# Kernel tuning notes

Measured on AMD Instinct MI355X. Metric: run time of the kernel, lower is better.

The kernel has to match this reference:

```python
import jax, jax.numpy as jnp
import numpy as np

NUM_QUBITS = 21
NUM_LAYERS = 4
ACTION_DIM = 18
STATE_DIM = 2 ** NUM_QUBITS  # amplitude register size


def _rx(t):
    c = jnp.cos(t / 2)
    s = jnp.sin(t / 2)
    return jnp.stack([jnp.stack([c + 0j, -1j * s]), jnp.stack([-1j * s, c + 0j])]).astype(jnp.complex64)


def _ry(t):
    c = jnp.cos(t / 2)
    s = jnp.sin(t / 2)
    return jnp.stack([jnp.stack([c, -s]), jnp.stack([s, c])]).astype(jnp.complex64)


def _rz(t):
    e = jnp.exp(-1j * t / 2).astype(jnp.complex64)
    z = jnp.zeros_like(e)
    return jnp.stack([jnp.stack([e, z]), jnp.stack([z, jnp.conj(e)])])


def apply_1q(psi, U, q):
    # wire 0 is the most-significant bit (PennyLane convention)
    s = psi.reshape(2 ** q, 2, -1)
    s = jnp.einsum('ab,xbz->xaz', U, s)
    return s.reshape(-1)


def apply_cnot(psi, c, t):
    a, b = (c, t) if c < t else (t, c)
    s = psi.reshape(2 ** a, 2, 2 ** (b - a - 1), 2, -1)
    ctrl_ax = 1 if c < t else 3
    tgt_ax = 3 if c < t else 1
    s0 = jax.lax.index_in_dim(s, 0, axis=ctrl_ax, keepdims=False)
    s1 = jax.lax.index_in_dim(s, 1, axis=ctrl_ax, keepdims=False)
    tgt_in_slab = tgt_ax if tgt_ax < ctrl_ax else tgt_ax - 1
    s1 = jnp.flip(s1, axis=tgt_in_slab)  # X on target where control==1
    s = jnp.stack([s0, s1], axis=ctrl_ax)
    return s.reshape(-1)


def _layer(psi, lp, entangle):
    # lp: (NUM_QUBITS, 3) rotation angles for this layer
    for q in range(NUM_QUBITS):
        psi = apply_1q(psi, _rx(lp[q, 0]), q)
        psi = apply_1q(psi, _ry(lp[q, 1]), q)
        psi = apply_1q(psi, _rz(lp[q, 2]), q)
    if entangle:
        for q in range(NUM_QUBITS - 1):
            psi = apply_cnot(psi, q, q + 1)
        psi = apply_cnot(psi, NUM_QUBITS - 1, 0)
    return psi


def setup_inputs() -> dict:
    key = jax.random.key(0)
    k1, k2, k3, k4 = jax.random.split(key, 4)
    state = jax.random.normal(k1, (STATE_DIM,), dtype=jnp.float32)
    circuit_params = jax.random.normal(k2, (NUM_LAYERS * NUM_QUBITS * 3,), dtype=jnp.float32) * 0.01
    bound = 1.0 / np.sqrt(NUM_QUBITS)
    head_w = jax.random.uniform(k3, (ACTION_DIM, NUM_QUBITS), jnp.float32, -bound, bound)
    head_b = jax.random.uniform(k4, (ACTION_DIM,), jnp.float32, -bound, bound)
    return {'state': state, 'circuit_params': circuit_params, 'head_w': head_w, 'head_b': head_b}


def reference(state, circuit_params, head_w, head_b):
    # Amplitude encoding: normalize (state_dim == 2**num_qubits so no padding needed)
    norm = jnp.linalg.norm(state)
    inv = jnp.where(norm > 0, 1.0 / jnp.maximum(norm, 1e-30), 0.0)
    basis0 = jnp.zeros((STATE_DIM,), jnp.float32).at[0].set(1.0)
    amp = jnp.where(norm > 0, state * inv, basis0)
    psi = amp.astype(jnp.complex64)

    lp = circuit_params.reshape(NUM_LAYERS, NUM_QUBITS, 3)
    for layer in range(NUM_LAYERS):
        psi = _layer(psi, lp[layer], layer < NUM_LAYERS - 1)

    # Pauli-Z expectation values per qubit from |psi|^2
    probs = psi.real ** 2 + psi.imag ** 2
    zvals = []
    for q in range(NUM_QUBITS):
        p = probs.reshape(2 ** q, 2, -1)
        zvals.append(p[:, 0, :].sum() - p[:, 1, :].sum())
    meas = jnp.stack(zvals).astype(jnp.float32)

    logits = head_w @ meas + head_b
    return jax.nn.softmax(logits, axis=-1)
```

## Files before the change

### kernel.cpp

```cpp
#include <hip/hip_runtime.h>

#define NQ 21
#define DIM (1 << NQ)
#define NL 4
#define ADIM 18
#define GBA 512
#define GBB 256
#define NT 512

__device__ __forceinline__ float2 cfma2(float2 u0, float2 a, float2 u1, float2 b) {
    return make_float2(u0.x * a.x - u0.y * a.y + u1.x * b.x - u1.y * b.y,
                       u0.x * a.y + u0.y * a.x + u1.x * b.y + u1.y * b.x);
}

struct GateU { float2 u00, u01, u10, u11; };

__device__ __forceinline__ void bfly(float2& a, float2& b, const GateU& U) {
    float2 na = cfma2(U.u00, a, U.u01, b);
    float2 nb = cfma2(U.u10, a, U.u11, b);
    a = na; b = nb;
}

__device__ __forceinline__ int sw(int j) { return j ^ (((j >> 4) & 7) << 1); }

__device__ __forceinline__ void make_mats(GateU* mats, const float* __restrict__ cp, int layer, int tid) {
    if (tid < NQ) {
        const float* ang = cp + (layer * NQ + tid) * 3;
        float a = ang[0], b = ang[1], c = ang[2];
        float ca = cosf(0.5f * a), sa = sinf(0.5f * a);
        float cb = cosf(0.5f * b), sb = sinf(0.5f * b);
        float cc = cosf(0.5f * c), sc = sinf(0.5f * c);
        float2 m00 = make_float2(cb * ca,  sb * sa);
        float2 m01 = make_float2(-sb * ca, -cb * sa);
        float2 m10 = make_float2(sb * ca,  -cb * sa);
        float2 m11 = make_float2(cb * ca,  -sb * sa);
        GateU U;
        U.u00 = make_float2(cc * m00.x + sc * m00.y, cc * m00.y - sc * m00.x);
        U.u01 = make_float2(cc * m01.x + sc * m01.y, cc * m01.y - sc * m01.x);
        U.u10 = make_float2(cc * m10.x - sc * m10.y, cc * m10.y + sc * m10.x);
        U.u11 = make_float2(cc * m11.x - sc * m11.y, cc * m11.y + sc * m11.x);
        mats[tid] = U;
    }
}

__device__ __forceinline__ void round3(float2* tile, int tid, int g,
                                       GateU Ua, GateU Ub, GateU Uc) {
    int bl = (1 << g) - 1;
    int base = (tid & bl) | ((tid >> g) << (g + 3));
    float2 v[8];
#pragma unroll
    for (int j = 0; j < 8; ++j) v[j] = tile[sw(base + (j << g))];
#pragma unroll
    for (int s = 0; s < 8; s += 2) bfly(v[s], v[s + 1], Ua);
#pragma unroll
    for (int s = 0; s < 8; ++s) if (!(s & 2)) bfly(v[s], v[s | 2], Ub);
#pragma unroll
    for (int s = 0; s < 8; ++s) if (!(s & 4)) bfly(v[s], v[s | 4], Uc);
#pragma unroll
    for (int j = 0; j < 8; ++j) tile[sw(base + (j << g))] = v[j];
    __syncthreads();
}

__global__ __launch_bounds__(NT, 4) void k_passB(const float* __restrict__ state,
                                                 float2* __restrict__ psi,
                                                 const float* __restrict__ cp, int layer) {
    __shared__ float2 tile[4096];
    __shared__ GateU mats[NQ];
    const int tid = threadIdx.x, blk = blockIdx.x;
    float4* psi4 = (float4*)psi;

    make_mats(mats, cp, layer, tid);
    const int srcmask = (layer < 3) ? 0xFF : 0;

    for (int H = 0; H < 2; ++H) {
        if (H) __syncthreads();
        if (layer == 0) {
            const float4* s4 = (const float4*)state;
            for (int i = 0; i < 2; ++i) {
                int f = i * NT + tid;
                int d = f & 1, h = f >> 1;
                float4 w = s4[(h << 10) | (blk << 2) | (2 * H + d)];
                int s = (h << 3) | (4 * d);
                tile[sw(s)]     = make_float2(w.x, 0.f);
                tile[sw(s + 1)] = make_float2(w.y, 0.f);
                tile[sw(s + 2)] = make_float2(w.z, 0.f);
                tile[sw(s + 3)] = make_float2(w.w, 0.f);
            }
        } else {
            for (int i = 0; i < 4; ++i) {
                int f = i * NT + tid;
                int c = f & 3, h = f >> 2;
                float4 w = psi4[(h << 11) | (blk << 3) | (4 * H + c)];
                int se = (h << 3) | (2 * c);
                tile[sw(se)]            = make_float2(w.x, w.y);
                tile[sw((se + 1) ^ 2048)] = make_float2(w.z, w.w);
            }
        }
        __syncthreads();
        round3(tile, tid, 3, mats[8], mats[7], mats[6]);
        round3(tile, tid, 6, mats[5], mats[4], mats[3]);
        round3(tile, tid, 9, mats[2], mats[1], mats[0]);
        for (int i = 0; i < 4; ++i) {
            int f = i * NT + tid;
            int c = f & 3, h = f >> 2;
            int hs = h ^ ((h >> 1) & srcmask);
            int s = (hs << 3) | (2 * c);
            float2 e0 = tile[sw(s)], e1 = tile[sw(s + 1)];
            psi4[(h << 11) | (blk << 3) | (4 * H + c)] = make_float4(e0.x, e0.y, e1.x, e1.y);
        }
    }
}

__global__ __launch_bounds__(NT, 4) void k_passA(float2* __restrict__ psi,
                                                 const float* __restrict__ cp, int layer,
                                                 float* __restrict__ partials) {
    __shared__ float2 tile[4096];
    __shared__ GateU mats[NQ];
    const int tid = threadIdx.x, blk = blockIdx.x;
    float4* psi4 = (float4*)psi;
    float4* t4 = (float4*)tile;

    {
        const float4* ga = psi4 + (size_t)blk * 2048;
        float2 v[8];
        float4 w[4];
        for (int i = 0; i < 4; ++i) w[i] = ga[i * NT + tid];
        make_mats(mats, cp, layer, tid);
        __syncthreads();
#pragma unroll
        for (int i = 0; i < 4; ++i) {
            v[2 * i]     = make_float2(w[i].x, w[i].y);
            v[2 * i + 1] = make_float2(w[i].z, w[i].w);
        }
        GateU U20 = mats[20];
#pragma unroll
        for (int s = 0; s < 8; s += 2) bfly(v[s], v[s + 1], U20);
        GateU U10 = mats[10];
#pragma unroll
        for (int s = 0; s < 8; ++s) if (!(s & 2)) bfly(v[s], v[s | 2], U10);
        GateU U9 = mats[9];
#pragma unroll
        for (int s = 0; s < 8; ++s) if (!(s & 4)) bfly(v[s], v[s | 4], U9);
        for (int i = 0; i < 4; ++i)
            t4[sw(2 * (i * NT + tid)) >> 1] =
                make_float4(v[2 * i].x, v[2 * i].y, v[2 * i + 1].x, v[2 * i + 1].y);
    }
    __syncthreads();
    round3(tile, tid, 1, mats[19], mats[18], mats[17]);
    round3(tile, tid, 4, mats[16], mats[15], mats[14]);
    round3(tile, tid, 7, mats[13], mats[12], mats[11]);

    if (layer < 3) {
        float4* oa = psi4 + (size_t)blk * 2048;
        int cb = (blk & 1) << 11;
        for (int i = 0; i < 4; ++i) {
            int f = i * NT + tid;
            int s0 = ((2 * f) ^ (f & 0x7FF)) ^ cb;
            float2 e0 = tile[sw(s0)], e1 = tile[sw(s0 ^ 1)];
            oa[f] = make_float4(e0.x, e0.y, e1.x, e1.y);
        }
    } else {
        float tot = 0.f, ones[NQ];
#pragma unroll
        for (int q = 0; q < NQ; ++q) ones[q] = 0.f;
        for (int it = 0; it < 8; ++it) {
            int j = it * NT + tid;
            float2 a2 = tile[sw(j)];
            float pr = a2.x * a2.x + a2.y * a2.y;
            int gidx = (blk << 12) | j;
            tot += pr;
#pragma unroll
            for (int q = 0; q < NQ; ++q)
                ones[q] += pr * (float)((gidx >> (20 - q)) & 1);
        }
        for (int off = 32; off; off >>= 1) {
            tot += __shfl_down(tot, off, 64);
#pragma unroll
            for (int q = 0; q < NQ; ++q) ones[q] += __shfl_down(ones[q], off, 64);
        }
        __syncthreads();
        float* red = (float*)tile;
        int wv = tid >> 6, ln = tid & 63;
        if (ln == 0) {
            red[wv * 22 + 21] = tot;
#pragma unroll
            for (int q = 0; q < NQ; ++q) red[wv * 22 + q] = ones[q];
        }
        __syncthreads();
        if (tid < 22) {
            float s = 0.f;
            for (int wvi = 0; wvi < 8; ++wvi) s += red[wvi * 22 + tid];
            partials[blk * 22 + tid] = s;
        }
    }
}

__global__ __launch_bounds__(NT) void k_final(const float* __restrict__ partials,
                                              const float* __restrict__ head_w,
                                              const float* __restrict__ head_b,
                                              float* __restrict__ out) {
    __shared__ float red[640];
    __shared__ float meas[NQ];
    __shared__ float lg[ADIM];
    int tid = threadIdx.x;
    int col = tid % 22, grp = tid / 22;
    if (tid < 506) {
        float s = 0.f;
        for (int r = grp; r < GBA; r += 23) s += partials[r * 22 + col];
        red[grp * 22 + col] = s;
    }
    __syncthreads();
    if (tid < 22) {
        float t2 = 0.f;
        for (int g = 0; g < 23; ++g) t2 += red[g * 22 + tid];
        red[600 + tid] = t2;
    }
    __syncthreads();
    if (tid < NQ) {
        float tot = red[600 + 21];
        meas[tid] = (tot > 0.f) ? (1.f - 2.f * red[600 + tid] / tot) : 1.f;
    }
    __syncthreads();
    if (tid < ADIM) {
        float s2 = head_b[tid];
        for (int q = 0; q < NQ; ++q) s2 += head_w[tid * NQ + q] * meas[q];
        lg[tid] = s2;
    }
    __syncthreads();
    if (tid == 0) {
        float m = lg[0];
        for (int a = 1; a < ADIM; ++a) m = fmaxf(m, lg[a]);
        float ssum = 0.f;
        for (int a = 0; a < ADIM; ++a) ssum += expf(lg[a] - m);
        float inv = 1.f / ssum;
        for (int a = 0; a < ADIM; ++a) out[a] = expf(lg[a] - m) * inv;
    }
}

extern "C" void kernel_launch(void* const* d_in, const int* in_sizes, int n_in,
                              void* d_out, int out_size, void* d_ws, size_t ws_size,
                              hipStream_t stream) {
    const float* state   = (const float*)d_in[0];
    const float* cparams = (const float*)d_in[1];
    const float* head_w  = (const float*)d_in[2];
    const float* head_b  = (const float*)d_in[3];
    float* out = (float*)d_out;

    float2* psi      = (float2*)d_ws;
    float*  partials = (float*)((char*)d_ws + (size_t)DIM * 8);

    for (int layer = 0; layer < NL; ++layer) {
        k_passB<<<GBB, NT, 0, stream>>>(state, psi, cparams, layer);
        k_passA<<<GBA, NT, 0, stream>>>(psi, cparams, layer, partials);
    }
    k_final<<<1, NT, 0, stream>>>(partials, head_w, head_b, out);
}
```

Baseline: 214.9 us.

## Prefetch both halves into registers, double-buffer LDS, fuse final reduction via last-block

Both passes now issue all global loads for a block's two tiles up front and keep two shared-memory buffers. This lets the second tile's memory latency overlap the first tile's butterfly rounds, and pass A runs half as many blocks, each doing two tiles. The separate final softmax kernel is removed: the last block to finish, detected with an atomic counter and cache-bypassing stores and loads, performs the reduction and head. Shared memory per block doubles and occupancy drops to 2 blocks per CU, and a memset launch is added.

Result: faster. 197.6 us (-8.1%).

```diff
diff --git a/kernel.cpp b/kernel.cpp
--- a/kernel.cpp
+++ b/kernel.cpp
@@ -4,8 +4,7 @@
 #define DIM (1 << NQ)
 #define NL 4
 #define ADIM 18
-#define GBA 512
-#define GBB 256
+#define GB 256
 #define NT 512
 
 __device__ __forceinline__ float2 cfma2(float2 u0, float2 a, float2 u1, float2 b) {
@@ -22,6 +21,19 @@
 }
 
 __device__ __forceinline__ int sw(int j) { return j ^ (((j >> 4) & 7) << 1); }
+
+__device__ __forceinline__ void store4_sc(float* p, float v) {
+    asm volatile("global_store_dword %0, %1, off sc0 sc1" :: "v"(p), "v"(v) : "memory");
+}
+__device__ __forceinline__ float load_sc_f(const float* p) {
+    float r;
+    asm volatile("global_load_dword %0, %1, off sc0 sc1\n\ts_waitcnt vmcnt(0)"
+                 : "=v"(r) : "v"(p) : "memory");
+    return r;
+}
+__device__ __forceinline__ void drain_vmem() {
+    asm volatile("s_waitcnt vmcnt(0)" ::: "memory");
+}
 
 __device__ __forceinline__ void make_mats(GateU* mats, const float* __restrict__ cp, int layer, int tid) {
     if (tid < NQ) {
@@ -61,125 +73,200 @@
     __syncthreads();
 }
 
-__global__ __launch_bounds__(NT, 4) void k_passB(const float* __restrict__ state,
+__global__ __launch_bounds__(NT, 2) void k_passB(const float* __restrict__ state,
                                                  float2* __restrict__ psi,
                                                  const float* __restrict__ cp, int layer) {
-    __shared__ float2 tile[4096];
+    __shared__ float2 tA[4096], tB[4096];
     __shared__ GateU mats[NQ];
     const int tid = threadIdx.x, blk = blockIdx.x;
     float4* psi4 = (float4*)psi;
-
+    const int srcmask = (layer < 3) ? 0xFF : 0;
+
+    float4 wA[4], wB[4];
+    if (layer == 0) {
+        const float4* s4 = (const float4*)state;
+        for (int i = 0; i < 2; ++i) {
+            int f = i * NT + tid, d = f & 1, h = f >> 1;
+            wA[i] = s4[(h << 10) | (blk << 2) | d];
+            wB[i] = s4[(h << 10) | (blk << 2) | (2 + d)];
+        }
+    } else {
+        for (int i = 0; i < 4; ++i) {
+            int f = i * NT + tid, c = f & 3, h = f >> 2;
+            wA[i] = psi4[(h << 11) | (blk << 3) | c];
+            wB[i] = psi4[(h << 11) | (blk << 3) | (4 + c)];
+        }
+    }
     make_mats(mats, cp, layer, tid);
-    const int srcmask = (layer < 3) ? 0xFF : 0;
-
-    for (int H = 0; H < 2; ++H) {
-        if (H) __syncthreads();
-        if (layer == 0) {
-            const float4* s4 = (const float4*)state;
-            for (int i = 0; i < 2; ++i) {
-                int f = i * NT + tid;
-                int d = f & 1, h = f >> 1;
-                float4 w = s4[(h << 10) | (blk << 2) | (2 * H + d)];
-                int s = (h << 3) | (4 * d);
-                tile[sw(s)]     = make_float2(w.x, 0.f);
-                tile[sw(s + 1)] = make_float2(w.y, 0.f);
-                tile[sw(s + 2)] = make_float2(w.z, 0.f);
-                tile[sw(s + 3)] = make_float2(w.w, 0.f);
-            }
-        } else {
-            for (int i = 0; i < 4; ++i) {
-                int f = i * NT + tid;
-                int c = f & 3, h = f >> 2;
-                float4 w = psi4[(h << 11) | (blk << 3) | (4 * H + c)];
-                int se = (h << 3) | (2 * c);
-                tile[sw(se)]            = make_float2(w.x, w.y);
-                tile[sw((se + 1) ^ 2048)] = make_float2(w.z, w.w);
-            }
-        }
-        __syncthreads();
-        round3(tile, tid, 3, mats[8], mats[7], mats[6]);
-        round3(tile, tid, 6, mats[5], mats[4], mats[3]);
-        round3(tile, tid, 9, mats[2], mats[1], mats[0]);
+    __syncthreads();
+
+    if (layer == 0) {
+        float4* t4 = (float4*)tA;
+        for (int i = 0; i < 2; ++i) {
+            int f = i * NT + tid, d = f & 1, h = f >> 1;
+            int j = (h << 3) | (4 * d);
+            float4 w = wA[i];
+            t4[sw(j) >> 1]     = make_float4(w.x, 0.f, w.y, 0.f);
+            t4[sw(j + 2) >> 1] = make_float4(w.z, 0.f, w.w, 0.f);
+        }
+    } else {
         for (int i = 0; i < 4; ++i) {
-            int f = i * NT + tid;
-            int c = f & 3, h = f >> 2;
-            int hs = h ^ ((h >> 1) & srcmask);
-            int s = (hs << 3) | (2 * c);
-            float2 e0 = tile[sw(s)], e1 = tile[sw(s + 1)];
-            psi4[(h << 11) | (blk << 3) | (4 * H + c)] = make_float4(e0.x, e0.y, e1.x, e1.y);
-        }
-    }
-}
-
-__global__ __launch_bounds__(NT, 4) void k_passA(float2* __restrict__ psi,
-                                                 const float* __restrict__ cp, int layer,
-                                                 float* __restrict__ partials) {
-    __shared__ float2 tile[4096];
-    __shared__ GateU mats[NQ];
-    const int tid = threadIdx.x, blk = blockIdx.x;
-    float4* psi4 = (float4*)psi;
+            int f = i * NT + tid, c = f & 3, h = f >> 2;
+            int se = (h << 3) | (2 * c);
+            float4 w = wA[i];
+            tA[sw(se)]              = make_float2(w.x, w.y);
+            tA[sw((se + 1) ^ 2048)] = make_float2(w.z, w.w);
+        }
+    }
+    __syncthreads();
+    round3(tA, tid, 3, mats[8], mats[7], mats[6]);
+    round3(tA, tid, 6, mats[5], mats[4], mats[3]);
+    round3(tA, tid, 9, mats[2], mats[1], mats[0]);
+
+    for (int i = 0; i < 4; ++i) {
+        int f = i * NT + tid, c = f & 3, h = f >> 2;
+        int hs = h ^ ((h >> 1) & srcmask);
+        int s = (hs << 3) | (2 * c);
+        float2 e0 = tA[sw(s)], e1 = tA[sw(s + 1)];
+        psi4[(h << 11) | (blk << 3) | c] = make_float4(e0.x, e0.y, e1.x, e1.y);
+    }
+    if (layer == 0) {
+        float4* t4 = (float4*)tB;
+        for (int i = 0; i < 2; ++i) {
+            int f = i * NT + tid, d = f & 1, h = f >> 1;
+            int j = (h << 3) | (4 * d);
+            float4 w = wB[i];
+            t4[sw(j) >> 1]     = make_float4(w.x, 0.f, w.y, 0.f);
+            t4[sw(j + 2) >> 1] = make_float4(w.z, 0.f, w.w, 0.f);
+        }
+    } else {
+        for (int i = 0; i < 4; ++i) {
+            int f = i * NT + tid, c = f & 3, h = f >> 2;
+            int se = (h << 3) | (2 * c);
+            float4 w = wB[i];
+            tB[sw(se)]              = make_float2(w.x, w.y);
+            tB[sw((se + 1) ^ 2048)] = make_float2(w.z, w.w);
+        }
+    }
+    __syncthreads();
+    round3(tB, tid, 3, mats[8], mats[7], mats[6]);
+    round3(tB, tid, 6, mats[5], mats[4], mats[3]);
+    round3(tB, tid, 9, mats[2], mats[1], mats[0]);
+    for (int i = 0; i < 4; ++i) {
+        int f = i * NT + tid, c = f & 3, h = f >> 2;
+        int hs = h ^ ((h >> 1) & srcmask);
+        int s = (hs << 3) | (2 * c);
+        float2 e0 = tB[sw(s)], e1 = tB[sw(s + 1)];
+        psi4[(h << 11) | (blk << 3) | (4 + c)] = make_float4(e0.x, e0.y, e1.x, e1.y);
+    }
+}
+
+__device__ __forceinline__ void a_regscatter(float2* tile, const float4* w,
+                                             const GateU* mats, int tid) {
+    float2 v[8];
     float4* t4 = (float4*)tile;
-
-    {
-        const float4* ga = psi4 + (size_t)blk * 2048;
-        float2 v[8];
-        float4 w[4];
-        for (int i = 0; i < 4; ++i) w[i] = ga[i * NT + tid];
-        make_mats(mats, cp, layer, tid);
-        __syncthreads();
-#pragma unroll
-        for (int i = 0; i < 4; ++i) {
-            v[2 * i]     = make_float2(w[i].x, w[i].y);
-            v[2 * i + 1] = make_float2(w[i].z, w[i].w);
-        }
-        GateU U20 = mats[20];
-#pragma unroll
-        for (int s = 0; s < 8; s += 2) bfly(v[s], v[s + 1], U20);
-        GateU U10 = mats[10];
-#pragma unroll
-        for (int s = 0; s < 8; ++s) if (!(s & 2)) bfly(v[s], v[s | 2], U10);
-        GateU U9 = mats[9];
-#pragma unroll
-        for (int s = 0; s < 8; ++s) if (!(s & 4)) bfly(v[s], v[s | 4], U9);
-        for (int i = 0; i < 4; ++i)
-            t4[sw(2 * (i * NT + tid)) >> 1] =
-                make_float4(v[2 * i].x, v[2 * i].y, v[2 * i + 1].x, v[2 * i + 1].y);
-    }
-    __syncthreads();
+#pragma unroll
+    for (int i = 0; i < 4; ++i) {
+        v[2 * i]     = make_float2(w[i].x, w[i].y);
+        v[2 * i + 1] = make_float2(w[i].z, w[i].w);
+    }
+    GateU U20 = mats[20];
+#pragma unroll
+    for (int s = 0; s < 8; s += 2) bfly(v[s], v[s + 1], U20);
+    GateU U10 = mats[10];
+#pragma unroll
+    for (int s = 0; s < 8; ++s) if (!(s & 2)) bfly(v[s], v[s | 2], U10);
+    GateU U9 = mats[9];
+#pragma unroll
+    for (int s = 0; s < 8; ++s) if (!(s & 4)) bfly(v[s], v[s | 4], U9);
+    for (int i = 0; i < 4; ++i)
+        t4[sw(2 * (i * NT + tid)) >> 1] =
+            make_float4(v[2 * i].x, v[2 * i].y, v[2 * i + 1].x, v[2 * i + 1].y);
+}
+
+__device__ __forceinline__ void a_rounds(float2* tile, const GateU* mats, int tid) {
     round3(tile, tid, 1, mats[19], mats[18], mats[17]);
     round3(tile, tid, 4, mats[16], mats[15], mats[14]);
     round3(tile, tid, 7, mats[13], mats[12], mats[11]);
+}
+
+__device__ __forceinline__ void a_gatherstore(float2* tile, float4* oa, int t, int tid) {
+    int cb = (t & 1) << 11;
+    for (int i = 0; i < 4; ++i) {
+        int f = i * NT + tid;
+        int s0 = ((2 * f) ^ (f & 0x7FF)) ^ cb;
+        float2 e0 = tile[sw(s0)], e1 = tile[sw(s0 ^ 1)];
+        oa[f] = make_float4(e0.x, e0.y, e1.x, e1.y);
+    }
+}
+
+__device__ __forceinline__ void a_accum(float2* tile, int t, int tid,
+                                        float& tot, float* ones) {
+    for (int it = 0; it < 8; ++it) {
+        int j = it * NT + tid;
+        float2 a2 = tile[sw(j)];
+        float pr = a2.x * a2.x + a2.y * a2.y;
+        int gidx = (t << 12) | j;
+        tot += pr;
+#pragma unroll
+        for (int q = 0; q < NQ; ++q)
+            ones[q] += pr * (float)((gidx >> (20 - q)) & 1);
+    }
+}
+
+__global__ __launch_bounds__(NT, 2) void k_passA(float2* __restrict__ psi,
+                                                 const float* __restrict__ cp, int layer,
+                                                 float* __restrict__ partials,
+                                                 const float* __restrict__ head_w,
+                                                 const float* __restrict__ head_b,
+                                                 float* __restrict__ out,
+                                                 int* __restrict__ done) {
+    __shared__ float2 tA[4096], tB[4096];
+    __shared__ GateU mats[NQ];
+    __shared__ float meas[NQ];
+    __shared__ float lg[ADIM];
+    __shared__ int lastflag;
+    const int tid = threadIdx.x, blk = blockIdx.x;
+    float4* psi4 = (float4*)psi;
+    const int t0 = 2 * blk, t1 = 2 * blk + 1;
+
+    float4 w0[4], w1[4];
+    {
+        const float4* ga0 = psi4 + (size_t)t0 * 2048;
+        const float4* ga1 = psi4 + (size_t)t1 * 2048;
+        for (int i = 0; i < 4; ++i) w0[i] = ga0[i * NT + tid];
+        for (int i = 0; i < 4; ++i) w1[i] = ga1[i * NT + tid];
+    }
+    make_mats(mats, cp, layer, tid);
+    __syncthreads();
+
+    a_regscatter(tA, w0, mats, tid);
+    __syncthreads();
+    a_rounds(tA, mats, tid);
 
     if (layer < 3) {
-        float4* oa = psi4 + (size_t)blk * 2048;
-        int cb = (blk & 1) << 11;
-        for (int i = 0; i < 4; ++i) {
-            int f = i * NT + tid;
-            int s0 = ((2 * f) ^ (f & 0x7FF)) ^ cb;
-            float2 e0 = tile[sw(s0)], e1 = tile[sw(s0 ^ 1)];
-            oa[f] = make_float4(e0.x, e0.y, e1.x, e1.y);
-        }
+        a_gatherstore(tA, psi4 + (size_t)t0 * 2048, t0, tid);
+        a_regscatter(tB, w1, mats, tid);
+        __syncthreads();
+        a_rounds(tB, mats, tid);
+        a_gatherstore(tB, psi4 + (size_t)t1 * 2048, t1, tid);
     } else {
         float tot = 0.f, ones[NQ];
 #pragma unroll
         for (int q = 0; q < NQ; ++q) ones[q] = 0.f;
-        for (int it = 0; it < 8; ++it) {
-            int j = it * NT + tid;
-            float2 a2 = tile[sw(j)];
-            float pr = a2.x * a2.x + a2.y * a2.y;
-            int gidx = (blk << 12) | j;
-            tot += pr;
-#pragma unroll
-            for (int q = 0; q < NQ; ++q)
-                ones[q] += pr * (float)((gidx >> (20 - q)) & 1);
-        }
+        a_accum(tA, t0, tid, tot, ones);
+        a_regscatter(tB, w1, mats, tid);
+        __syncthreads();
+        a_rounds(tB, mats, tid);
+        a_accum(tB, t1, tid, tot, ones);
+
         for (int off = 32; off; off >>= 1) {
             tot += __shfl_down(tot, off, 64);
 #pragma unroll
             for (int q = 0; q < NQ; ++q) ones[q] += __shfl_down(ones[q], off, 64);
         }
         __syncthreads();
-        float* red = (float*)tile;
+        float* red = (float*)tA;
         int wv = tid >> 6, ln = tid & 63;
         if (ln == 0) {
             red[wv * 22 + 21] = tot;
@@ -190,50 +277,47 @@
         if (tid < 22) {
             float s = 0.f;
             for (int wvi = 0; wvi < 8; ++wvi) s += red[wvi * 22 + tid];
-            partials[blk * 22 + tid] = s;
-        }
-    }
-}
-
-__global__ __launch_bounds__(NT) void k_final(const float* __restrict__ partials,
-                                              const float* __restrict__ head_w,
-                                              const float* __restrict__ head_b,
-                                              float* __restrict__ out) {
-    __shared__ float red[640];
-    __shared__ float meas[NQ];
-    __shared__ float lg[ADIM];
-    int tid = threadIdx.x;
-    int col = tid % 22, grp = tid / 22;
-    if (tid < 506) {
-        float s = 0.f;
-        for (int r = grp; r < GBA; r += 23) s += partials[r * 22 + col];
-        red[grp * 22 + col] = s;
-    }
-    __syncthreads();
-    if (tid < 22) {
-        float t2 = 0.f;
-        for (int g = 0; g < 23; ++g) t2 += red[g * 22 + tid];
-        red[600 + tid] = t2;
-    }
-    __syncthreads();
-    if (tid < NQ) {
-        float tot = red[600 + 21];
-        meas[tid] = (tot > 0.f) ? (1.f - 2.f * red[600 + tid] / tot) : 1.f;
-    }
-    __syncthreads();
-    if (tid < ADIM) {
-        float s2 = head_b[tid];
-        for (int q = 0; q < NQ; ++q) s2 += head_w[tid * NQ + q] * meas[q];
-        lg[tid] = s2;
-    }
-    __syncthreads();
-    if (tid == 0) {
-        float m = lg[0];
-        for (int a = 1; a < ADIM; ++a) m = fmaxf(m, lg[a]);
-        float ssum = 0.f;
-        for (int a = 0; a < ADIM; ++a) ssum += expf(lg[a] - m);
-        float inv = 1.f / ssum;
-        for (int a = 0; a < ADIM; ++a) out[a] = expf(lg[a] - m) * inv;
+            store4_sc(&partials[blk * 22 + tid], s);
+        }
+        drain_vmem();
+        __syncthreads();
+        if (tid == 0) lastflag = (atomicAdd(done, 1) == GB - 1);
+        __syncthreads();
+        if (!lastflag) return;
+
+        float* red2 = (float*)tB;
+        int col = tid % 22, grp = tid / 22;
+        if (tid < 506) {
+            float s = 0.f;
+            for (int r = grp; r < GB; r += 23) s += load_sc_f(&partials[r * 22 + col]);
+            red2[grp * 22 + col] = s;
+        }
+        __syncthreads();
+        if (tid < 22) {
+            float t2 = 0.f;
+            for (int g = 0; g < 23; ++g) t2 += red2[g * 22 + tid];
+            red2[600 + tid] = t2;
+        }
+        __syncthreads();
+        if (tid < NQ) {
+            float tt = red2[600 + 21];
+            meas[tid] = (tt > 0.f) ? (1.f - 2.f * red2[600 + tid] / tt) : 1.f;
+        }
+        __syncthreads();
+        if (tid < ADIM) {
+            float s2 = head_b[tid];
+            for (int q = 0; q < NQ; ++q) s2 += head_w[tid * NQ + q] * meas[q];
+            lg[tid] = s2;
+        }
+        __syncthreads();
+        if (tid == 0) {
+            float m = lg[0];
+            for (int a = 1; a < ADIM; ++a) m = fmaxf(m, lg[a]);
+            float ssum = 0.f;
+            for (int a = 0; a < ADIM; ++a) ssum += expf(lg[a] - m);
+            float inv = 1.f / ssum;
+            for (int a = 0; a < ADIM; ++a) out[a] = expf(lg[a] - m) * inv;
+        }
     }
 }
 
@@ -246,12 +330,15 @@
     const float* head_b  = (const float*)d_in[3];
     float* out = (float*)d_out;
 
-    float2* psi      = (float2*)d_ws;
-    float*  partials = (float*)((char*)d_ws + (size_t)DIM * 8);
-
+    char* ws = (char*)d_ws;
+    float2* psi      = (float2*)ws;
+    float*  partials = (float*)(ws + (size_t)DIM * 8);
+    int*    done     = (int*)(ws + (size_t)DIM * 8 + 32768);
+
+    hipMemsetAsync(done, 0, 4, stream);
     for (int layer = 0; layer < NL; ++layer) {
-        k_passB<<<GBB, NT, 0, stream>>>(state, psi, cparams, layer);
-        k_passA<<<GBA, NT, 0, stream>>>(psi, cparams, layer, partials);
-    }
-    k_final<<<1, NT, 0, stream>>>(partials, head_w, head_b, out);
-}
+        k_passB<<<GB, NT, 0, stream>>>(state, psi, cparams, layer);
+        k_passA<<<GB, NT, 0, stream>>>(psi, cparams, layer, partials,
+                                       head_w, head_b, out, done);
+    }
+}
```

## Split passB halves across blocks and fuse final reduction via last-block atomic

Applied to the files above, without the earlier changes.

Pass B now launches 512 blocks, each handling one of the two halves that a block previously processed in a serial loop, which doubles parallelism and removes an in-block sync. The separate final kernel is removed: the last pass-A block to finish, found with an atomic counter, reduces the partials and computes the softmax head. Partials are written and read with cache-bypassing sc0/sc1 inline asm so the last block sees the other blocks' results. The layer-0 state load into the tile also uses wider float4 shared stores. Risks are the extra atomic and fence work in every block of the final layer.

After: 214.5 us. Within noise of the previous version (-0.2%).

```diff
diff --git a/kernel.cpp b/kernel.cpp
--- a/kernel.cpp
+++ b/kernel.cpp
@@ -4,8 +4,7 @@
 #define DIM (1 << NQ)
 #define NL 4
 #define ADIM 18
-#define GBA 512
-#define GBB 256
+#define GB 512
 #define NT 512
 
 __device__ __forceinline__ float2 cfma2(float2 u0, float2 a, float2 u1, float2 b) {
@@ -22,6 +21,19 @@
 }
 
 __device__ __forceinline__ int sw(int j) { return j ^ (((j >> 4) & 7) << 1); }
+
+__device__ __forceinline__ void store4_sc(float* p, float v) {
+    asm volatile("global_store_dword %0, %1, off sc0 sc1" :: "v"(p), "v"(v) : "memory");
+}
+__device__ __forceinline__ float load_sc_f(const float* p) {
+    float r;
+    asm volatile("global_load_dword %0, %1, off sc0 sc1\n\ts_waitcnt vmcnt(0)"
+                 : "=v"(r) : "v"(p) : "memory");
+    return r;
+}
+__device__ __forceinline__ void drain_vmem() {
+    asm volatile("s_waitcnt vmcnt(0)" ::: "memory");
+}
 
 __device__ __forceinline__ void make_mats(GateU* mats, const float* __restrict__ cp, int layer, int tid) {
     if (tid < NQ) {
@@ -63,92 +75,115 @@
 
 __global__ __launch_bounds__(NT, 4) void k_passB(const float* __restrict__ state,
                                                  float2* __restrict__ psi,
-                                                 const float* __restrict__ cp, int layer) {
+                                                 const float* __restrict__ cp, int layer,
+                                                 int* __restrict__ done) {
     __shared__ float2 tile[4096];
     __shared__ GateU mats[NQ];
     const int tid = threadIdx.x, blk = blockIdx.x;
+    const int blkB = blk >> 1, H = blk & 1;
     float4* psi4 = (float4*)psi;
+    const int srcmask = (layer < 3) ? 0xFF : 0;
 
     make_mats(mats, cp, layer, tid);
-    const int srcmask = (layer < 3) ? 0xFF : 0;
-
-    for (int H = 0; H < 2; ++H) {
-        if (H) __syncthreads();
-        if (layer == 0) {
-            const float4* s4 = (const float4*)state;
-            for (int i = 0; i < 2; ++i) {
-                int f = i * NT + tid;
-                int d = f & 1, h = f >> 1;
-                float4 w = s4[(h << 10) | (blk << 2) | (2 * H + d)];
-                int s = (h << 3) | (4 * d);
-                tile[sw(s)]     = make_float2(w.x, 0.f);
-                tile[sw(s + 1)] = make_float2(w.y, 0.f);
-                tile[sw(s + 2)] = make_float2(w.z, 0.f);
-                tile[sw(s + 3)] = make_float2(w.w, 0.f);
-            }
-        } else {
-            for (int i = 0; i < 4; ++i) {
-                int f = i * NT + tid;
-                int c = f & 3, h = f >> 2;
-                float4 w = psi4[(h << 11) | (blk << 3) | (4 * H + c)];
-                int se = (h << 3) | (2 * c);
-                tile[sw(se)]            = make_float2(w.x, w.y);
-                tile[sw((se + 1) ^ 2048)] = make_float2(w.z, w.w);
-            }
-        }
-        __syncthreads();
-        round3(tile, tid, 3, mats[8], mats[7], mats[6]);
-        round3(tile, tid, 6, mats[5], mats[4], mats[3]);
-        round3(tile, tid, 9, mats[2], mats[1], mats[0]);
+    if (layer == 0 && blk == 0 && tid == 32) *done = 0;
+    __syncthreads();
+
+    if (layer == 0) {
+        const float4* s4 = (const float4*)state;
+        float4 w[2];
+        for (int i = 0; i < 2; ++i) {
+            int f = i * NT + tid, d = f & 1, h = f >> 1;
+            w[i] = s4[(h << 10) | (blkB << 2) | (2 * H + d)];
+        }
+        float4* t4 = (float4*)tile;
+        for (int i = 0; i < 2; ++i) {
+            int f = i * NT + tid, d = f & 1, h = f >> 1;
+            int j = (h << 3) | (4 * d);
+            t4[sw(j) >> 1]     = make_float4(w[i].x, 0.f, w[i].y, 0.f);
+            t4[sw(j + 2) >> 1] = make_float4(w[i].z, 0.f, w[i].w, 0.f);
+        }
+    } else {
+        float4 w[4];
         for (int i = 0; i < 4; ++i) {
-            int f = i * NT + tid;
-            int c = f & 3, h = f >> 2;
-            int hs = h ^ ((h >> 1) & srcmask);
-            int s = (hs << 3) | (2 * c);
-            float2 e0 = tile[sw(s)], e1 = tile[sw(s + 1)];
-            psi4[(h << 11) | (blk << 3) | (4 * H + c)] = make_float4(e0.x, e0.y, e1.x, e1.y);
-        }
-    }
-}
-
-__global__ __launch_bounds__(NT, 4) void k_passA(float2* __restrict__ psi,
-                                                 const float* __restrict__ cp, int layer,
-                                                 float* __restrict__ partials) {
-    __shared__ float2 tile[4096];
-    __shared__ GateU mats[NQ];
-    const int tid = threadIdx.x, blk = blockIdx.x;
-    float4* psi4 = (float4*)psi;
+            int f = i * NT + tid, c = f & 3, h = f >> 2;
+            w[i] = psi4[(h << 11) | (blkB << 3) | (4 * H + c)];
+        }
+        for (int i = 0; i < 4; ++i) {
+            int f = i * NT + tid, c = f & 3, h = f >> 2;
+            int se = (h << 3) | (2 * c);
+            tile[sw(se)]              = make_float2(w[i].x, w[i].y);
+            tile[sw((se + 1) ^ 2048)] = make_float2(w[i].z, w[i].w);
+        }
+    }
+    __syncthreads();
+    round3(tile, tid, 3, mats[8], mats[7], mats[6]);
+    round3(tile, tid, 6, mats[5], mats[4], mats[3]);
+    round3(tile, tid, 9, mats[2], mats[1], mats[0]);
+    for (int i = 0; i < 4; ++i) {
+        int f = i * NT + tid, c = f & 3, h = f >> 2;
+        int hs = h ^ ((h >> 1) & srcmask);
+        int s = (hs << 3) | (2 * c);
+        float2 e0 = tile[sw(s)], e1 = tile[sw(s + 1)];
+        psi4[(h << 11) | (blkB << 3) | (4 * H + c)] = make_float4(e0.x, e0.y, e1.x, e1.y);
+    }
+}
+
+__device__ __forceinline__ void a_regscatter(float2* tile, const float4* w,
+                                             const GateU* mats, int tid) {
+    float2 v[8];
     float4* t4 = (float4*)tile;
-
-    {
-        const float4* ga = psi4 + (size_t)blk * 2048;
-        float2 v[8];
-        float4 w[4];
-        for (int i = 0; i < 4; ++i) w[i] = ga[i * NT + tid];
-        make_mats(mats, cp, layer, tid);
-        __syncthreads();
-#pragma unroll
-        for (int i = 0; i < 4; ++i) {
-            v[2 * i]     = make_float2(w[i].x, w[i].y);
-            v[2 * i + 1] = make_float2(w[i].z, w[i].w);
-        }
-        GateU U20 = mats[20];
-#pragma unroll
-        for (int s = 0; s < 8; s += 2) bfly(v[s], v[s + 1], U20);
-        GateU U10 = mats[10];
-#pragma unroll
-        for (int s = 0; s < 8; ++s) if (!(s & 2)) bfly(v[s], v[s | 2], U10);
-        GateU U9 = mats[9];
-#pragma unroll
-        for (int s = 0; s < 8; ++s) if (!(s & 4)) bfly(v[s], v[s | 4], U9);
-        for (int i = 0; i < 4; ++i)
-            t4[sw(2 * (i * NT + tid)) >> 1] =
-                make_float4(v[2 * i].x, v[2 * i].y, v[2 * i + 1].x, v[2 * i + 1].y);
-    }
-    __syncthreads();
+#pragma unroll
+    for (int i = 0; i < 4; ++i) {
+        v[2 * i]     = make_float2(w[i].x, w[i].y);
+        v[2 * i + 1] = make_float2(w[i].z, w[i].w);
+    }
+    GateU U20 = mats[20];
+#pragma unroll
+    for (int s = 0; s < 8; s += 2) bfly(v[s], v[s + 1], U20);
+    GateU U10 = mats[10];
+#pragma unroll
+    for (int s = 0; s < 8; ++s) if (!(s & 2)) bfly(v[s], v[s | 2], U10);
+    GateU U9 = mats[9];
+#pragma unroll
+    for (int s = 0; s < 8; ++s) if (!(s & 4)) bfly(v[s], v[s | 4], U9);
+    for (int i = 0; i < 4; ++i)
+        t4[sw(2 * (i * NT + tid)) >> 1] =
+            make_float4(v[2 * i].x, v[2 * i].y, v[2 * i + 1].x, v[2 * i + 1].y);
+}
+
+__device__ __forceinline__ void a_rounds(float2* tile, const GateU* mats, int tid) {
     round3(tile, tid, 1, mats[19], mats[18], mats[17]);
     round3(tile, tid, 4, mats[16], mats[15], mats[14]);
     round3(tile, tid, 7, mats[13], mats[12], mats[11]);
+}
+
+__global__ __launch_bounds__(NT, 4) void k_passA(float2* __restrict__ psi,
+                                                 const float* __restrict__ cp, int layer,
+                                                 float* __restrict__ partials,
+                                                 const float* __restrict__ head_w,
+                                                 const float* __restrict__ head_b,
+                                                 float* __restrict__ out,
+                                                 int* __restrict__ done) {
+    __shared__ float2 tile[4096];
+    __shared__ GateU mats[NQ];
+    __shared__ float red2[640];
+    __shared__ float meas[NQ];
+    __shared__ float lg[ADIM];
+    __shared__ int lastflag;
+    const int tid = threadIdx.x, blk = blockIdx.x;
+    float4* psi4 = (float4*)psi;
+
+    make_mats(mats, cp, layer, tid);
+    __syncthreads();
+
+    float4 w[4];
+    {
+        const float4* ga = psi4 + (size_t)blk * 2048;
+        for (int i = 0; i < 4; ++i) w[i] = ga[i * NT + tid];
+    }
+    a_regscatter(tile, w, mats, tid);
+    __syncthreads();
+    a_rounds(tile, mats, tid);
 
     if (layer < 3) {
         float4* oa = psi4 + (size_t)blk * 2048;
@@ -190,50 +225,46 @@
         if (tid < 22) {
             float s = 0.f;
             for (int wvi = 0; wvi < 8; ++wvi) s += red[wvi * 22 + tid];
-            partials[blk * 22 + tid] = s;
-        }
-    }
-}
-
-__global__ __launch_bounds__(NT) void k_final(const float* __restrict__ partials,
-                                              const float* __restrict__ head_w,
-                                              const float* __restrict__ head_b,
-                                              float* __restrict__ out) {
-    __shared__ float red[640];
-    __shared__ float meas[NQ];
-    __shared__ float lg[ADIM];
-    int tid = threadIdx.x;
-    int col = tid % 22, grp = tid / 22;
-    if (tid < 506) {
-        float s = 0.f;
-        for (int r = grp; r < GBA; r += 23) s += partials[r * 22 + col];
-        red[grp * 22 + col] = s;
-    }
-    __syncthreads();
-    if (tid < 22) {
-        float t2 = 0.f;
-        for (int g = 0; g < 23; ++g) t2 += red[g * 22 + tid];
-        red[600 + tid] = t2;
-    }
-    __syncthreads();
-    if (tid < NQ) {
-        float tot = red[600 + 21];
-        meas[tid] = (tot > 0.f) ? (1.f - 2.f * red[600 + tid] / tot) : 1.f;
-    }
-    __syncthreads();
-    if (tid < ADIM) {
-        float s2 = head_b[tid];
-        for (int q = 0; q < NQ; ++q) s2 += head_w[tid * NQ + q] * meas[q];
-        lg[tid] = s2;
-    }
-    __syncthreads();
-    if (tid == 0) {
-        float m = lg[0];
-        for (int a = 1; a < ADIM; ++a) m = fmaxf(m, lg[a]);
-        float ssum = 0.f;
-        for (int a = 0; a < ADIM; ++a) ssum += expf(lg[a] - m);
-        float inv = 1.f / ssum;
-        for (int a = 0; a < ADIM; ++a) out[a] = expf(lg[a] - m) * inv;
+            store4_sc(&partials[blk * 22 + tid], s);
+        }
+        drain_vmem();
+        __syncthreads();
+        if (tid == 0) lastflag = (atomicAdd(done, 1) == GB - 1);
+        __syncthreads();
+        if (!lastflag) return;
+
+        int col = tid % 22, grp = tid / 22;
+        if (tid < 506) {
+            float s = 0.f;
+            for (int r = grp; r < GB; r += 23) s += load_sc_f(&partials[r * 22 + col]);
+            red2[grp * 22 + col] = s;
+        }
+        __syncthreads();
+        if (tid < 22) {
+            float t2 = 0.f;
+            for (int g = 0; g < 23; ++g) t2 += red2[g * 22 + tid];
+            red2[600 + tid] = t2;
+        }
+        __syncthreads();
+        if (tid < NQ) {
+            float tt = red2[600 + 21];
+            meas[tid] = (tt > 0.f) ? (1.f - 2.f * red2[600 + tid] / tt) : 1.f;
+        }
+        __syncthreads();
+        if (tid < ADIM) {
+            float s2 = head_b[tid];
+            for (int q = 0; q < NQ; ++q) s2 += head_w[tid * NQ + q] * meas[q];
+            lg[tid] = s2;
+        }
+        __syncthreads();
+        if (tid == 0) {
+            float m = lg[0];
+            for (int a = 1; a < ADIM; ++a) m = fmaxf(m, lg[a]);
+            float ssum = 0.f;
+            for (int a = 0; a < ADIM; ++a) ssum += expf(lg[a] - m);
+            float inv = 1.f / ssum;
+            for (int a = 0; a < ADIM; ++a) out[a] = expf(lg[a] - m) * inv;
+        }
     }
 }
 
@@ -246,12 +277,14 @@
     const float* head_b  = (const float*)d_in[3];
     float* out = (float*)d_out;
 
-    float2* psi      = (float2*)d_ws;
-    float*  partials = (float*)((char*)d_ws + (size_t)DIM * 8);
+    char* ws = (char*)d_ws;
+    float2* psi      = (float2*)ws;
+    float*  partials = (float*)(ws + (size_t)DIM * 8);
+    int*    done     = (int*)(ws + (size_t)DIM * 8 + 49152);
 
     for (int layer = 0; layer < NL; ++layer) {
-        k_passB<<<GBB, NT, 0, stream>>>(state, psi, cparams, layer);
-        k_passA<<<GBA, NT, 0, stream>>>(psi, cparams, layer, partials);
-    }
-    k_final<<<1, NT, 0, stream>>>(partials, head_w, head_b, out);
-}
+        k_passB<<<GB, NT, 0, stream>>>(state, psi, cparams, layer, done);
+        k_passA<<<GB, NT, 0, stream>>>(psi, cparams, layer, partials,
+                                       head_w, head_b, out, done);
+    }
+}
```
